# Optimization experiments

Measured on AMD Instinct MI355X. Metric: run time of the kernel, lower is better.

## Reference

```python
import jax, jax.numpy as jnp
import numpy as np
import math

D_HEAD = 64
EPS = 1e-6


def _rms_norm(x, scale, eps):
    # compute in float32 like the torch reference (promote_types with float32)
    xf = x.astype(jnp.float32)
    ms = jnp.mean(xf * xf, axis=-1, keepdims=True)
    return (xf * (scale.astype(jnp.float32) * jax.lax.rsqrt(ms + eps))).astype(x.dtype)


def _apply_rotary(x, cos, sin):
    # rotate first 2*cos_dim channels, pass the rest through
    ro = cos.shape[-1] * 2
    xr, xp = x[..., :ro], x[..., ro:]
    c = jnp.concatenate([cos, cos], axis=-1)
    s = jnp.concatenate([sin, sin], axis=-1)
    x1, x2 = jnp.split(xr, 2, axis=-1)
    rot = jnp.concatenate([-x2, x1], axis=-1)
    return jnp.concatenate([xr * c + rot * s, xp], axis=-1)


def _nb_idx(L, k):
    # NATTEN neighborhood start: window of size k clamped inside [0, L)
    i = jnp.arange(L)
    start = jnp.clip(i - k // 2, 0, L - k)
    return start[:, None] + jnp.arange(k)[None, :]  # [L, k]


def setup_inputs() -> dict:
    key = jax.random.key(0)
    ks = jax.random.split(key, 6)
    n, H, W, d_model, cond_features = 2, 48, 48, 256, 256
    x = jax.random.normal(ks[0], (n, H, W, d_model), dtype=jnp.float32)
    axis = jnp.linspace(-1.0, 1.0, H, dtype=jnp.float32)
    gh, gw = jnp.meshgrid(axis, axis, indexing='ij')
    pos = jnp.stack([gh, gw], axis=-1)  # [H, W, 2]
    cond = jax.random.normal(ks[1], (n, cond_features), dtype=jnp.float32)
    w_norm = jax.random.normal(ks[2], (d_model, cond_features), dtype=jnp.float32) * 0.01
    w_qkv = jax.random.normal(ks[3], (3 * d_model, d_model), dtype=jnp.float32) / math.sqrt(d_model)
    w_out = jax.random.normal(ks[4], (d_model, d_model), dtype=jnp.float32) * 0.02
    return {"x": x, "pos": pos, "cond": cond, "w_norm": w_norm, "w_qkv": w_qkv,
            "w_out": w_out, "kernel_size": 7}


def reference(x, pos, cond, w_norm, w_qkv, w_out, kernel_size):
    n, H, W, d_model = x.shape
    e = D_HEAD
    nh = d_model // e
    k = kernel_size
    skip = x

    # AdaRMSNorm: scale = linear(cond) + 1, broadcast over h, w
    scale = (cond @ w_norm.T)[:, None, None, :] + 1.0  # [n,1,1,d_model]
    xn = _rms_norm(x, scale, EPS)

    # QKV projection -> [3, n, nh, H, W, e]
    qkv = (xn @ w_qkv.T).reshape(n, H, W, 3, nh, e)
    qkv = jnp.transpose(qkv, (3, 0, 4, 1, 2, 5))
    q, kk, v = qkv[0], qkv[1], qkv[2]

    # Axial RoPE: freqs buffer of AxialRoPE(d_head // 2)
    dim = e // 2
    nf = dim // 4
    freqs = jnp.exp(jnp.linspace(math.log(math.pi), math.log(10.0 * math.pi), nf + 1)[:-1]).astype(jnp.float32)
    fh = pos[..., 0:1] * freqs  # [H,W,nf]
    fw = pos[..., 1:2] * freqs
    fr = jnp.concatenate([fh, fw], axis=-1)  # [H,W,2*nf] == [H,W,e//4]
    cos, sin = jnp.cos(fr), jnp.sin(fr)
    q = _apply_rotary(q, cos, sin)
    kk = _apply_rotary(kk, cos, sin)
    q = q / math.sqrt(e)

    # 2D neighborhood attention (natten2dqk / natten2dav, dilation 1)
    idx_h = _nb_idx(H, k)  # [H,k]
    idx_w = _nb_idx(W, k)  # [W,k]
    kg = kk[:, :, idx_h][:, :, :, :, idx_w]  # [n,nh,H,k,W,k,e]
    vg = v[:, :, idx_h][:, :, :, :, idx_w]   # [n,nh,H,k,W,k,e]
    qk = jnp.einsum('bmije,bmipjqe->bmijpq', q, kg).reshape(n, nh, H, W, k * k)
    a = jax.nn.softmax(qk, axis=-1).reshape(n, nh, H, W, k, k)
    o = jnp.einsum('bmijpq,bmipjqe->bmije', a, vg)  # [n,nh,H,W,e]

    o = jnp.transpose(o, (0, 2, 3, 1, 4)).reshape(n, H, W, d_model)
    return o @ w_out.T + skip
```

## Files before the change

kernel.cpp:

```cpp
#include <hip/hip_runtime.h>
#include <math.h>

#define N_B 2
#define HH 48
#define WW 48
#define DM 256
#define NH 4
#define EH 64
#define KS 7
#define NPIX (N_B*HH*WW)
#define NQ   (N_B*NH*HH*WW)

typedef _Float16 half8 __attribute__((ext_vector_type(8)));
typedef float float4v __attribute__((ext_vector_type(4)));

__global__ void scale_kernel(const float* __restrict__ cond,
                             const float* __restrict__ w_norm,
                             float* __restrict__ scale) {
    int b = blockIdx.x, d = threadIdx.x;
    __shared__ float csh[DM];
    csh[d] = cond[b*DM + d];
    __syncthreads();
    const float* wr = w_norm + (size_t)d*DM;
    float acc = 0.f;
    #pragma unroll 8
    for (int c = 0; c < DM; ++c) acc += csh[c]*wr[c];
    scale[b*DM + d] = acc + 1.0f;
}

__global__ void rmsnorm_kernel(const float* __restrict__ x,
                               const float* __restrict__ scale,
                               _Float16* __restrict__ xn) {
    int pix = blockIdx.x, t = threadIdx.x;
    int b = pix / (HH*WW);
    float v = x[(size_t)pix*DM + t];
    float ss = v*v;
    #pragma unroll
    for (int off = 32; off > 0; off >>= 1) ss += __shfl_xor(ss, off, 64);
    __shared__ float wsum[4];
    if ((t & 63) == 0) wsum[t>>6] = ss;
    __syncthreads();
    float tot = wsum[0]+wsum[1]+wsum[2]+wsum[3];
    float r = rsqrtf(tot*(1.0f/DM) + 1e-6f);
    xn[(size_t)pix*DM + t] = (_Float16)(v * scale[b*DM + t] * r);
}

__global__ void cast_f16_kernel(const float* __restrict__ src, _Float16* __restrict__ dst, int n) {
    int i = blockIdx.x*256 + threadIdx.x;
    if (i < n) dst[i] = (_Float16)src[i];
}

__global__ __launch_bounds__(256) void gemm_qkv_f16(const _Float16* __restrict__ A,
                                                    const _Float16* __restrict__ B,
                                                    const float* __restrict__ pos,
                                                    _Float16* __restrict__ qh,
                                                    _Float16* __restrict__ kh,
                                                    _Float16* __restrict__ vh) {
    const int K = DM;
    const int LDT = 40;
    __shared__ _Float16 As[128*LDT];
    __shared__ _Float16 Bs[64*LDT];
    int t = threadIdx.x;
    int wave = t >> 6, lane = t & 63;
    int m0 = blockIdx.x*128, n0 = blockIdx.y*64;

    int lr = t >> 2;
    int lk = (t & 3) * 8;

    float4v acc[2][4];
    #pragma unroll
    for (int mi = 0; mi < 2; ++mi)
        #pragma unroll
        for (int ni = 0; ni < 4; ++ni)
            acc[mi][ni] = (float4v){0.f,0.f,0.f,0.f};

    int frow = lane & 15;
    int kq   = (lane >> 4) * 8;

    for (int k0 = 0; k0 < K; k0 += 32) {
        half8 a0 = *(const half8*)(A + (size_t)(m0 + lr)*K      + k0 + lk);
        half8 a1 = *(const half8*)(A + (size_t)(m0 + 64 + lr)*K + k0 + lk);
        half8 b0 = *(const half8*)(B + (size_t)(n0 + lr)*K      + k0 + lk);
        __syncthreads();
        *(half8*)&As[lr*LDT + lk]      = a0;
        *(half8*)&As[(64+lr)*LDT + lk] = a1;
        *(half8*)&Bs[lr*LDT + lk]      = b0;
        __syncthreads();
        half8 af[2], bf[4];
        af[0] = *(const half8*)&As[(wave*32 + frow)*LDT + kq];
        af[1] = *(const half8*)&As[(wave*32 + 16 + frow)*LDT + kq];
        #pragma unroll
        for (int ni = 0; ni < 4; ++ni)
            bf[ni] = *(const half8*)&Bs[(ni*16 + frow)*LDT + kq];
        #pragma unroll
        for (int mi = 0; mi < 2; ++mi)
            #pragma unroll
            for (int ni = 0; ni < 4; ++ni)
                acc[mi][ni] = __builtin_amdgcn_mfma_f32_16x16x32_f16(af[mi], bf[ni], acc[mi][ni], 0, 0, 0);
    }

    int sel  = n0 >> 8;
    int head = (n0 >> 6) & 3;
    _Float16* outp = (sel == 0) ? qh : (sel == 1) ? kh : vh;
    int col   = lane & 15;
    int rbase = (lane >> 4) * 4;
    float freq = __expf(1.14472988585f + (float)(col & 7) * 0.287823136624f);
    #pragma unroll
    for (int mi = 0; mi < 2; ++mi) {
        #pragma unroll
        for (int r = 0; r < 4; ++r) {
            int pix = m0 + wave*32 + mi*16 + rbase + r;
            float v0 = acc[mi][0][r], v1 = acc[mi][1][r];
            float v2 = acc[mi][2][r], v3 = acc[mi][3][r];
            if (sel < 2) {
                int hw = pix % (HH*WW);
                float p = (col < 8) ? pos[hw*2] : pos[hw*2+1];
                float sn, cs;
                __sincosf(p*freq, &sn, &cs);
                float o0 = v0*cs - v1*sn;
                float o1 = v1*cs + v0*sn;
                v0 = o0; v1 = o1;
                if (sel == 0) { v0*=0.125f; v1*=0.125f; v2*=0.125f; v3*=0.125f; }
            }
            size_t base = (size_t)pix*DM + head*EH;
            outp[base +  0 + col] = (_Float16)v0;
            outp[base + 16 + col] = (_Float16)v1;
            outp[base + 32 + col] = (_Float16)v2;
            outp[base + 48 + col] = (_Float16)v3;
        }
    }
}

__global__ __launch_bounds__(256) void attn_mfma(const _Float16* __restrict__ qg,
                                                 const _Float16* __restrict__ kg,
                                                 const _Float16* __restrict__ vg,
                                                 _Float16* __restrict__ obuf) {
    __shared__ _Float16 VT[64*232];
    __shared__ _Float16 SP[64*232];
    int t = threadIdx.x;
    int wave = t >> 6, lane = t & 63;
    int col = lane & 15, quad = lane >> 4;
    int ty = blockIdx.x / 6, tx = blockIdx.x % 6;
    int b = blockIdx.y >> 2, head = blockIdx.y & 3;
    int qh0 = ty*8, qw0 = tx*8;
    int rh0 = min(max(qh0-3, 0), HH-14);
    int rw0 = min(max(qw0-3, 0), WW-14);

    {
        int nbl = t & 31;
        int e0  = (t >> 5) * 8;
        #pragma unroll
        for (int pass = 0; pass < 7; ++pass) {
            int nb = pass*32 + nbl;
            int nr = nb >> 4, nc = nb & 15;
            int pix = (b*HH + rh0+nr)*WW + rw0 + nc;
            half8 vv = *(const half8*)(vg + (size_t)pix*DM + head*EH + e0);
            #pragma unroll
            for (int i = 0; i < 8; ++i)
                VT[(e0+i)*232 + nb] = vv[i];
        }
    }

    int qidx_a = wave*16 + col;
    int pixq = (b*HH + qh0 + (qidx_a>>3))*WW + qw0 + (qidx_a & 7);
    const _Float16* qp = qg + (size_t)pixq*DM + head*EH;
    half8 qf0 = *(const half8*)(qp + quad*8);
    half8 qf1 = *(const half8*)(qp + 32 + quad*8);

    float4v s[14];
    #pragma unroll
    for (int nr = 0; nr < 14; ++nr) {
        int pixk = (b*HH + rh0+nr)*WW + rw0 + col;
        const _Float16* kp = kg + (size_t)pixk*DM + head*EH;
        half8 kf0 = *(const half8*)(kp + quad*8);
        half8 kf1 = *(const half8*)(kp + 32 + quad*8);
        float4v a = (float4v){0.f,0.f,0.f,0.f};
        a = __builtin_amdgcn_mfma_f32_16x16x32_f16(qf0, kf0, a, 0, 0, 0);
        a = __builtin_amdgcn_mfma_f32_16x16x32_f16(qf1, kf1, a, 0, 0, 0);
        s[nr] = a;
    }

    int sh_[4], uw_[4];
    #pragma unroll
    for (int r = 0; r < 4; ++r) {
        int qidx = wave*16 + quad*4 + r;
        int qhh = qh0 + (qidx>>3), qww = qw0 + (qidx & 7);
        sh_[r] = min(max(qhh-3, 0), HH-KS);
        int sw_ = min(max(qww-3, 0), WW-KS);
        uw_[r] = rw0 + col - sw_;
    }
    #pragma unroll
    for (int nr = 0; nr < 14; ++nr)
        #pragma unroll
        for (int r = 0; r < 4; ++r) {
            int uh = rh0 + nr - sh_[r];
            bool ok = ((unsigned)uh < 7u) && ((unsigned)uw_[r] < 7u);
            s[nr][r] = ok ? s[nr][r] : -1e30f;
        }
    #pragma unroll
    for (int r = 0; r < 4; ++r) {
        float m = s[0][r];
        #pragma unroll
        for (int nr = 1; nr < 14; ++nr) m = fmaxf(m, s[nr][r]);
        m = fmaxf(m, __shfl_xor(m, 1, 64));
        m = fmaxf(m, __shfl_xor(m, 2, 64));
        m = fmaxf(m, __shfl_xor(m, 4, 64));
        m = fmaxf(m, __shfl_xor(m, 8, 64));
        float sum = 0.f;
        #pragma unroll
        for (int nr = 0; nr < 14; ++nr) { float p = __expf(s[nr][r] - m); s[nr][r] = p; sum += p; }
        sum += __shfl_xor(sum, 1, 64);
        sum += __shfl_xor(sum, 2, 64);
        sum += __shfl_xor(sum, 4, 64);
        sum += __shfl_xor(sum, 8, 64);
        float rs = 1.f / sum;
        #pragma unroll
        for (int nr = 0; nr < 14; ++nr)
            SP[(wave*16 + quad*4 + r)*232 + nr*16 + col] = (_Float16)(s[nr][r] * rs);
    }
    __syncthreads();

    float4v o[4];
    #pragma unroll
    for (int dt = 0; dt < 4; ++dt) o[dt] = (float4v){0.f,0.f,0.f,0.f};
    #pragma unroll
    for (int ks = 0; ks < 7; ++ks) {
        half8 pa = *(const half8*)&SP[(wave*16 + col)*232 + ks*32 + quad*8];
        #pragma unroll
        for (int dt = 0; dt < 4; ++dt) {
            half8 vf = *(const half8*)&VT[(dt*16 + col)*232 + ks*32 + quad*8];
            o[dt] = __builtin_amdgcn_mfma_f32_16x16x32_f16(pa, vf, o[dt], 0, 0, 0);
        }
    }
    #pragma unroll
    for (int r = 0; r < 4; ++r) {
        int qidx = wave*16 + quad*4 + r;
        int pix = (b*HH + qh0 + (qidx>>3))*WW + qw0 + (qidx & 7);
        #pragma unroll
        for (int dt = 0; dt < 4; ++dt)
            obuf[(size_t)pix*DM + head*EH + dt*16 + col] = (_Float16)o[dt][r];
    }
}

__global__ __launch_bounds__(256) void gemm_nt_f16(const _Float16* __restrict__ A,
                                                   const _Float16* __restrict__ B,
                                                   float* __restrict__ C,
                                                   const float* __restrict__ skip,
                                                   int M, int N, int K) {
    const int LDT = 40;
    __shared__ _Float16 As[128*LDT];
    __shared__ _Float16 Bs[64*LDT];
    int t = threadIdx.x;
    int wave = t >> 6, lane = t & 63;
    int m0 = blockIdx.x*128, n0 = blockIdx.y*64;

    int lr = t >> 2;
    int lk = (t & 3) * 8;

    float4v acc[2][4];
    #pragma unroll
    for (int mi = 0; mi < 2; ++mi)
        #pragma unroll
        for (int ni = 0; ni < 4; ++ni)
            acc[mi][ni] = (float4v){0.f,0.f,0.f,0.f};

    int frow = lane & 15;
    int kq   = (lane >> 4) * 8;

    for (int k0 = 0; k0 < K; k0 += 32) {
        half8 a0 = *(const half8*)(A + (size_t)(m0 + lr)*K      + k0 + lk);
        half8 a1 = *(const half8*)(A + (size_t)(m0 + 64 + lr)*K + k0 + lk);
        half8 b0 = *(const half8*)(B + (size_t)(n0 + lr)*K      + k0 + lk);
        __syncthreads();
        *(half8*)&As[lr*LDT + lk]      = a0;
        *(half8*)&As[(64+lr)*LDT + lk] = a1;
        *(half8*)&Bs[lr*LDT + lk]      = b0;
        __syncthreads();
        half8 af[2], bf[4];
        af[0] = *(const half8*)&As[(wave*32 + frow)*LDT + kq];
        af[1] = *(const half8*)&As[(wave*32 + 16 + frow)*LDT + kq];
        #pragma unroll
        for (int ni = 0; ni < 4; ++ni)
            bf[ni] = *(const half8*)&Bs[(ni*16 + frow)*LDT + kq];
        #pragma unroll
        for (int mi = 0; mi < 2; ++mi)
            #pragma unroll
            for (int ni = 0; ni < 4; ++ni)
                acc[mi][ni] = __builtin_amdgcn_mfma_f32_16x16x32_f16(af[mi], bf[ni], acc[mi][ni], 0, 0, 0);
    }

    int col   = lane & 15;
    int rbase = (lane >> 4) * 4;
    #pragma unroll
    for (int mi = 0; mi < 2; ++mi) {
        #pragma unroll
        for (int ni = 0; ni < 4; ++ni) {
            #pragma unroll
            for (int r = 0; r < 4; ++r) {
                int row = m0 + wave*32 + mi*16 + rbase + r;
                int c   = n0 + ni*16 + col;
                float v = acc[mi][ni][r];
                if (skip) v += skip[(size_t)row*N + c];
                C[(size_t)row*N + c] = v;
            }
        }
    }
}

extern "C" void kernel_launch(void* const* d_in, const int* in_sizes, int n_in,
                              void* d_out, int out_size, void* d_ws, size_t ws_size,
                              hipStream_t stream) {
    const float* x      = (const float*)d_in[0];
    const float* pos    = (const float*)d_in[1];
    const float* cond   = (const float*)d_in[2];
    const float* w_norm = (const float*)d_in[3];
    const float* w_qkv  = (const float*)d_in[4];
    const float* w_out  = (const float*)d_in[5];
    float* out = (float*)d_out;
    char* base = (char*)d_ws;

    const size_t SZH = (size_t)NPIX*DM*2;
    const size_t PAD = 4096;
    float*    scale  = (float*)(base);
    _Float16* xn_h   = (_Float16*)(base + PAD);
    _Float16* qh     = (_Float16*)(base + PAD + 1*(SZH+PAD));
    _Float16* kh     = (_Float16*)(base + PAD + 2*(SZH+PAD));
    _Float16* vh     = (_Float16*)(base + PAD + 3*(SZH+PAD));
    _Float16* obuf_h = (_Float16*)(base + PAD + 4*(SZH+PAD));
    _Float16* wqkv_h = (_Float16*)(base + PAD + 5*(SZH+PAD));
    _Float16* wout_h = (_Float16*)(base + PAD + 5*(SZH+PAD) + 786432);

    scale_kernel<<<dim3(N_B), dim3(DM), 0, stream>>>(cond, w_norm, scale);
    rmsnorm_kernel<<<dim3(NPIX), dim3(DM), 0, stream>>>(x, scale, xn_h);
    cast_f16_kernel<<<dim3(768), dim3(256), 0, stream>>>(w_qkv, wqkv_h, 768*DM);
    cast_f16_kernel<<<dim3(256), dim3(256), 0, stream>>>(w_out, wout_h, DM*DM);
    gemm_qkv_f16<<<dim3(NPIX/128, 12), 256, 0, stream>>>(xn_h, wqkv_h, pos, qh, kh, vh);
    attn_mfma<<<dim3(36, N_B*NH), 256, 0, stream>>>(qh, kh, vh, obuf_h);
    gemm_nt_f16<<<dim3(NPIX/128, DM/64), 256, 0, stream>>>(obuf_h, wout_h, out, x, NPIX, DM, DM);
}
```

Before: 122.7 us.

## Fuse weight casts into GEMMs, shrink GEMM tiles, parallelize scale kernel

Removes the two separate fp32-to-fp16 weight cast kernels and has both GEMMs load fp32 weights directly and convert them while staging into shared memory. GEMM M-tiles shrink from 128 to 64 rows, doubling block count for better CU occupancy on this small problem. The scale kernel is spread over more blocks, with vectorized loads and a shuffle reduction. The trade-off is that each weight tile is re-read in fp32 and re-converted by every M-block, which raises weight traffic, and the smaller tiles give less data reuse per block.

```diff
diff --git a/kernel.cpp b/kernel.cpp
--- a/kernel.cpp
+++ b/kernel.cpp
@@ -9,7 +9,6 @@
 #define EH 64
 #define KS 7
 #define NPIX (N_B*HH*WW)
-#define NQ   (N_B*NH*HH*WW)
 
 typedef _Float16 half8 __attribute__((ext_vector_type(8)));
 typedef float float4v __attribute__((ext_vector_type(4)));
@@ -17,15 +16,22 @@
 __global__ void scale_kernel(const float* __restrict__ cond,
                              const float* __restrict__ w_norm,
                              float* __restrict__ scale) {
-    int b = blockIdx.x, d = threadIdx.x;
-    __shared__ float csh[DM];
-    csh[d] = cond[b*DM + d];
-    __syncthreads();
-    const float* wr = w_norm + (size_t)d*DM;
+    int b = blockIdx.x;
+    int t = threadIdx.x, wave = t >> 6, lane = t & 63;
+    int d = blockIdx.y*32 + wave*8 + (lane >> 3);
+    int l8 = lane & 7;
+    const float4* wr4 = (const float4*)(w_norm + (size_t)d*DM) + l8*8;
+    const float4* c4  = (const float4*)(cond + (size_t)b*DM) + l8*8;
     float acc = 0.f;
-    #pragma unroll 8
-    for (int c = 0; c < DM; ++c) acc += csh[c]*wr[c];
-    scale[b*DM + d] = acc + 1.0f;
+    #pragma unroll
+    for (int j = 0; j < 8; ++j) {
+        float4 w = wr4[j], c = c4[j];
+        acc += w.x*c.x + w.y*c.y + w.z*c.z + w.w*c.w;
+    }
+    acc += __shfl_xor(acc, 1, 64);
+    acc += __shfl_xor(acc, 2, 64);
+    acc += __shfl_xor(acc, 4, 64);
+    if (l8 == 0) scale[b*DM + d] = acc + 1.0f;
 }
 
 __global__ void rmsnorm_kernel(const float* __restrict__ x,
@@ -45,89 +51,70 @@
     xn[(size_t)pix*DM + t] = (_Float16)(v * scale[b*DM + t] * r);
 }
 
-__global__ void cast_f16_kernel(const float* __restrict__ src, _Float16* __restrict__ dst, int n) {
-    int i = blockIdx.x*256 + threadIdx.x;
-    if (i < n) dst[i] = (_Float16)src[i];
-}
-
 __global__ __launch_bounds__(256) void gemm_qkv_f16(const _Float16* __restrict__ A,
-                                                    const _Float16* __restrict__ B,
+                                                    const float* __restrict__ B,
                                                     const float* __restrict__ pos,
                                                     _Float16* __restrict__ qh,
                                                     _Float16* __restrict__ kh,
                                                     _Float16* __restrict__ vh) {
-    const int K = DM;
-    const int LDT = 40;
-    __shared__ _Float16 As[128*LDT];
+    const int K = DM, LDT = 40;
+    __shared__ _Float16 As[64*LDT];
     __shared__ _Float16 Bs[64*LDT];
     int t = threadIdx.x;
     int wave = t >> 6, lane = t & 63;
-    int m0 = blockIdx.x*128, n0 = blockIdx.y*64;
-
-    int lr = t >> 2;
-    int lk = (t & 3) * 8;
-
-    float4v acc[2][4];
-    #pragma unroll
-    for (int mi = 0; mi < 2; ++mi)
-        #pragma unroll
-        for (int ni = 0; ni < 4; ++ni)
-            acc[mi][ni] = (float4v){0.f,0.f,0.f,0.f};
-
-    int frow = lane & 15;
-    int kq   = (lane >> 4) * 8;
+    int m0 = blockIdx.x*64, n0 = blockIdx.y*64;
+    int lr = t >> 2, lk = (t & 3) * 8;
+
+    float4v acc[4];
+    #pragma unroll
+    for (int ni = 0; ni < 4; ++ni) acc[ni] = (float4v){0.f,0.f,0.f,0.f};
+
+    int frow = lane & 15, kq = (lane >> 4) * 8;
 
     for (int k0 = 0; k0 < K; k0 += 32) {
-        half8 a0 = *(const half8*)(A + (size_t)(m0 + lr)*K      + k0 + lk);
-        half8 a1 = *(const half8*)(A + (size_t)(m0 + 64 + lr)*K + k0 + lk);
-        half8 b0 = *(const half8*)(B + (size_t)(n0 + lr)*K      + k0 + lk);
+        half8 a0 = *(const half8*)(A + (size_t)(m0 + lr)*K + k0 + lk);
+        const float* bp = B + (size_t)(n0 + lr)*K + k0 + lk;
+        float4 b0 = *(const float4*)bp;
+        float4 b1 = *(const float4*)(bp + 4);
+        half8 hb;
+        hb[0]=(_Float16)b0.x; hb[1]=(_Float16)b0.y; hb[2]=(_Float16)b0.z; hb[3]=(_Float16)b0.w;
+        hb[4]=(_Float16)b1.x; hb[5]=(_Float16)b1.y; hb[6]=(_Float16)b1.z; hb[7]=(_Float16)b1.w;
         __syncthreads();
-        *(half8*)&As[lr*LDT + lk]      = a0;
-        *(half8*)&As[(64+lr)*LDT + lk] = a1;
-        *(half8*)&Bs[lr*LDT + lk]      = b0;
+        *(half8*)&As[lr*LDT + lk] = a0;
+        *(half8*)&Bs[lr*LDT + lk] = hb;
         __syncthreads();
-        half8 af[2], bf[4];
-        af[0] = *(const half8*)&As[(wave*32 + frow)*LDT + kq];
-        af[1] = *(const half8*)&As[(wave*32 + 16 + frow)*LDT + kq];
-        #pragma unroll
-        for (int ni = 0; ni < 4; ++ni)
-            bf[ni] = *(const half8*)&Bs[(ni*16 + frow)*LDT + kq];
-        #pragma unroll
-        for (int mi = 0; mi < 2; ++mi)
-            #pragma unroll
-            for (int ni = 0; ni < 4; ++ni)
-                acc[mi][ni] = __builtin_amdgcn_mfma_f32_16x16x32_f16(af[mi], bf[ni], acc[mi][ni], 0, 0, 0);
+        half8 af = *(const half8*)&As[(wave*16 + frow)*LDT + kq];
+        #pragma unroll
+        for (int ni = 0; ni < 4; ++ni) {
+            half8 bf = *(const half8*)&Bs[(ni*16 + frow)*LDT + kq];
+            acc[ni] = __builtin_amdgcn_mfma_f32_16x16x32_f16(af, bf, acc[ni], 0, 0, 0);
+        }
     }
 
     int sel  = n0 >> 8;
     int head = (n0 >> 6) & 3;
     _Float16* outp = (sel == 0) ? qh : (sel == 1) ? kh : vh;
-    int col   = lane & 15;
-    int rbase = (lane >> 4) * 4;
+    int col = lane & 15, rbase = (lane >> 4) * 4;
     float freq = __expf(1.14472988585f + (float)(col & 7) * 0.287823136624f);
     #pragma unroll
-    for (int mi = 0; mi < 2; ++mi) {
-        #pragma unroll
-        for (int r = 0; r < 4; ++r) {
-            int pix = m0 + wave*32 + mi*16 + rbase + r;
-            float v0 = acc[mi][0][r], v1 = acc[mi][1][r];
-            float v2 = acc[mi][2][r], v3 = acc[mi][3][r];
-            if (sel < 2) {
-                int hw = pix % (HH*WW);
-                float p = (col < 8) ? pos[hw*2] : pos[hw*2+1];
-                float sn, cs;
-                __sincosf(p*freq, &sn, &cs);
-                float o0 = v0*cs - v1*sn;
-                float o1 = v1*cs + v0*sn;
-                v0 = o0; v1 = o1;
-                if (sel == 0) { v0*=0.125f; v1*=0.125f; v2*=0.125f; v3*=0.125f; }
-            }
-            size_t base = (size_t)pix*DM + head*EH;
-            outp[base +  0 + col] = (_Float16)v0;
-            outp[base + 16 + col] = (_Float16)v1;
-            outp[base + 32 + col] = (_Float16)v2;
-            outp[base + 48 + col] = (_Float16)v3;
-        }
+    for (int r = 0; r < 4; ++r) {
+        int pix = m0 + wave*16 + rbase + r;
+        float v0 = acc[0][r], v1 = acc[1][r], v2 = acc[2][r], v3 = acc[3][r];
+        if (sel < 2) {
+            int hw = pix % (HH*WW);
+            float p = (col < 8) ? pos[hw*2] : pos[hw*2+1];
+            float sn, cs;
+            __sincosf(p*freq, &sn, &cs);
+            float o0 = v0*cs - v1*sn;
+            float o1 = v1*cs + v0*sn;
+            v0 = o0; v1 = o1;
+            if (sel == 0) { v0*=0.125f; v1*=0.125f; v2*=0.125f; v3*=0.125f; }
+        }
+        size_t base = (size_t)pix*DM + head*EH;
+        outp[base +  0 + col] = (_Float16)v0;
+        outp[base + 16 + col] = (_Float16)v1;
+        outp[base + 32 + col] = (_Float16)v2;
+        outp[base + 48 + col] = (_Float16)v3;
     }
 }
 
@@ -242,67 +229,52 @@
     }
 }
 
-__global__ __launch_bounds__(256) void gemm_nt_f16(const _Float16* __restrict__ A,
-                                                   const _Float16* __restrict__ B,
-                                                   float* __restrict__ C,
-                                                   const float* __restrict__ skip,
-                                                   int M, int N, int K) {
-    const int LDT = 40;
-    __shared__ _Float16 As[128*LDT];
+__global__ __launch_bounds__(256) void gemm_out_f16(const _Float16* __restrict__ A,
+                                                    const float* __restrict__ B,
+                                                    float* __restrict__ C,
+                                                    const float* __restrict__ skip) {
+    const int K = DM, N = DM, LDT = 40;
+    __shared__ _Float16 As[64*LDT];
     __shared__ _Float16 Bs[64*LDT];
     int t = threadIdx.x;
     int wave = t >> 6, lane = t & 63;
-    int m0 = blockIdx.x*128, n0 = blockIdx.y*64;
-
-    int lr = t >> 2;
-    int lk = (t & 3) * 8;
-
-    float4v acc[2][4];
-    #pragma unroll
-    for (int mi = 0; mi < 2; ++mi)
-        #pragma unroll
-        for (int ni = 0; ni < 4; ++ni)
-            acc[mi][ni] = (float4v){0.f,0.f,0.f,0.f};
-
-    int frow = lane & 15;
-    int kq   = (lane >> 4) * 8;
+    int m0 = blockIdx.x*64, n0 = blockIdx.y*64;
+    int lr = t >> 2, lk = (t & 3) * 8;
+
+    float4v acc[4];
+    #pragma unroll
+    for (int ni = 0; ni < 4; ++ni) acc[ni] = (float4v){0.f,0.f,0.f,0.f};
+
+    int frow = lane & 15, kq = (lane >> 4) * 8;
 
     for (int k0 = 0; k0 < K; k0 += 32) {
-        half8 a0 = *(const half8*)(A + (size_t)(m0 + lr)*K      + k0 + lk);
-        half8 a1 = *(const half8*)(A + (size_t)(m0 + 64 + lr)*K + k0 + lk);
-        half8 b0 = *(const half8*)(B + (size_t)(n0 + lr)*K      + k0 + lk);
+        half8 a0 = *(const half8*)(A + (size_t)(m0 + lr)*K + k0 + lk);
+        const float* bp = B + (size_t)(n0 + lr)*K + k0 + lk;
+        float4 b0 = *(const float4*)bp;
+        float4 b1 = *(const float4*)(bp + 4);
+        half8 hb;
+        hb[0]=(_Float16)b0.x; hb[1]=(_Float16)b0.y; hb[2]=(_Float16)b0.z; hb[3]=(_Float16)b0.w;
+        hb[4]=(_Float16)b1.x; hb[5]=(_Float16)b1.y; hb[6]=(_Float16)b1.z; hb[7]=(_Float16)b1.w;
         __syncthreads();
-        *(half8*)&As[lr*LDT + lk]      = a0;
-        *(half8*)&As[(64+lr)*LDT + lk] = a1;
-        *(half8*)&Bs[lr*LDT + lk]      = b0;
+        *(half8*)&As[lr*LDT + lk] = a0;
+        *(half8*)&Bs[lr*LDT + lk] = hb;
         __syncthreads();
-        half8 af[2], bf[4];
-        af[0] = *(const half8*)&As[(wave*32 + frow)*LDT + kq];
-        af[1] = *(const half8*)&As[(wave*32 + 16 + frow)*LDT + kq];
-        #pragma unroll
-        for (int ni = 0; ni < 4; ++ni)
-            bf[ni] = *(const half8*)&Bs[(ni*16 + frow)*LDT + kq];
-        #pragma unroll
-        for (int mi = 0; mi < 2; ++mi)
-            #pragma unroll
-            for (int ni = 0; ni < 4; ++ni)
-                acc[mi][ni] = __builtin_amdgcn_mfma_f32_16x16x32_f16(af[mi], bf[ni], acc[mi][ni], 0, 0, 0);
-    }
-
-    int col   = lane & 15;
-    int rbase = (lane >> 4) * 4;
-    #pragma unroll
-    for (int mi = 0; mi < 2; ++mi) {
+        half8 af = *(const half8*)&As[(wave*16 + frow)*LDT + kq];
         #pragma unroll
         for (int ni = 0; ni < 4; ++ni) {
-            #pragma unroll
-            for (int r = 0; r < 4; ++r) {
-                int row = m0 + wave*32 + mi*16 + rbase + r;
-                int c   = n0 + ni*16 + col;
-                float v = acc[mi][ni][r];
-                if (skip) v += skip[(size_t)row*N + c];
-                C[(size_t)row*N + c] = v;
-            }
+            half8 bf = *(const half8*)&Bs[(ni*16 + frow)*LDT + kq];
+            acc[ni] = __builtin_amdgcn_mfma_f32_16x16x32_f16(af, bf, acc[ni], 0, 0, 0);
+        }
+    }
+
+    int col = lane & 15, rbase = (lane >> 4) * 4;
+    #pragma unroll
+    for (int ni = 0; ni < 4; ++ni) {
+        #pragma unroll
+        for (int r = 0; r < 4; ++r) {
+            int row = m0 + wave*16 + rbase + r;
+            int c   = n0 + ni*16 + col;
+            C[(size_t)row*N + c] = acc[ni][r] + skip[(size_t)row*N + c];
         }
     }
 }
@@ -327,14 +299,10 @@
     _Float16* kh     = (_Float16*)(base + PAD + 2*(SZH+PAD));
     _Float16* vh     = (_Float16*)(base + PAD + 3*(SZH+PAD));
     _Float16* obuf_h = (_Float16*)(base + PAD + 4*(SZH+PAD));
-    _Float16* wqkv_h = (_Float16*)(base + PAD + 5*(SZH+PAD));
-    _Float16* wout_h = (_Float16*)(base + PAD + 5*(SZH+PAD) + 786432);
-
-    scale_kernel<<<dim3(N_B), dim3(DM), 0, stream>>>(cond, w_norm, scale);
+
+    scale_kernel<<<dim3(N_B, 8), 256, 0, stream>>>(cond, w_norm, scale);
     rmsnorm_kernel<<<dim3(NPIX), dim3(DM), 0, stream>>>(x, scale, xn_h);
-    cast_f16_kernel<<<dim3(768), dim3(256), 0, stream>>>(w_qkv, wqkv_h, 768*DM);
-    cast_f16_kernel<<<dim3(256), dim3(256), 0, stream>>>(w_out, wout_h, DM*DM);
-    gemm_qkv_f16<<<dim3(NPIX/128, 12), 256, 0, stream>>>(xn_h, wqkv_h, pos, qh, kh, vh);
+    gemm_qkv_f16<<<dim3(NPIX/64, 12), 256, 0, stream>>>(xn_h, w_qkv, pos, qh, kh, vh);
     attn_mfma<<<dim3(36, N_B*NH), 256, 0, stream>>>(qh, kh, vh, obuf_h);
-    gemm_nt_f16<<<dim3(NPIX/128, DM/64), 256, 0, stream>>>(obuf_h, wout_h, out, x, NPIX, DM, DM);
-}
+    gemm_out_f16<<<dim3(NPIX/64, DM/64), 256, 0, stream>>>(obuf_h, w_out, out, x);
+}
```

New measurement: 105.8 us. -13.8%, faster.
